# Performance work log

Hardware: AMD Instinct MI355X
Metric: run time of the kernel (lower is better)

The kernel has to match this reference:

```python
import jax, jax.numpy as jnp
import numpy as np
from math import sqrt

NUM_HEAD = 16
HEAD_DIM = 64  # out_dim // num_head = 1024 // 16


def setup_inputs() -> dict:
    key = jax.random.key(0)
    ks = jax.random.split(key, 6)
    B, L, D = 2, 2048, 1024
    s = 1.0 / sqrt(D)
    return {
        "x": jax.random.normal(ks[0], (B, L, D), jnp.float32),
        "position_embedding": jax.random.normal(ks[1], (1, NUM_HEAD, L, L), jnp.float32),
        "Wq": jax.random.normal(ks[2], (D, D), jnp.float32) * s,
        "Wk": jax.random.normal(ks[3], (D, D), jnp.float32) * s,
        "Wv": jax.random.normal(ks[4], (D, D), jnp.float32) * s,
        "Wo": jax.random.normal(ks[5], (D, D), jnp.float32) * s,
    }


def reference(x, position_embedding, Wq, Wk, Wv, Wo):
    # x: [B, L, D]; torch Linear(y = x @ W.T) -> here weights stored as [in, out]
    B, L, D = x.shape
    H, Hd = NUM_HEAD, HEAD_DIM
    q = (x @ Wq).reshape(B, L, H, Hd).transpose(0, 2, 1, 3)  # [B,H,L,Hd]
    k = (x @ Wk).reshape(B, L, H, Hd).transpose(0, 2, 1, 3)
    v = (x @ Wv).reshape(B, L, H, Hd).transpose(0, 2, 1, 3)
    scores = jnp.einsum("bhqd,bhkd->bhqk", q, k) / sqrt(Hd)  # [B,H,L,L]
    scores = scores + position_embedding
    attn = jax.nn.softmax(scores, axis=-1)
    out = jnp.einsum("bhqk,bhkd->bhqd", attn, v)  # [B,H,L,Hd]
    out = out.transpose(0, 2, 1, 3).reshape(B, L, H * Hd)
    return out @ Wo
```

## Files before the change

kernel.cpp:

```cpp
#include <hip/hip_runtime.h>
#include <hip/hip_bf16.h>
#include <stdint.h>

typedef __hip_bfloat16 bf16;
typedef __attribute__((ext_vector_type(8))) short bf16x8;
typedef __attribute__((ext_vector_type(4))) float f32x4;
typedef __attribute__((ext_vector_type(16))) float f32x16;
typedef __attribute__((ext_vector_type(4))) unsigned u32x4;

#define B_  2
#define L_  2048
#define D_  1024
#define H_  16
#define HD_ 64
#define BH_ 32
#define L2E 1.4426950408889634f

#define DEV static __device__ __forceinline__

DEV short f2bf(float f) {
    bf16 h = __float2bfloat16(f);
    return __builtin_bit_cast(short, h);
}

DEV unsigned pk2(float lo, float hi) {
    unsigned a = (unsigned short)__builtin_bit_cast(unsigned short, __float2bfloat16(lo));
    unsigned b = (unsigned short)__builtin_bit_cast(unsigned short, __float2bfloat16(hi));
    return a | (b << 16);
}

DEV f32x4 mfma16(bf16x8 a, bf16x8 b, f32x4 c) {
    return __builtin_amdgcn_mfma_f32_16x16x32_bf16(a, b, c, 0, 0, 0);
}
DEV f32x16 mfma32(bf16x8 a, bf16x8 b, f32x16 c) {
    return __builtin_amdgcn_mfma_f32_32x32x16_bf16(a, b, c, 0, 0, 0);
}

DEV void async_ld16(const void* g, void* lds_uniform) {
    __builtin_amdgcn_global_load_lds((const __attribute__((address_space(1))) void*)g,
                                     (__attribute__((address_space(3))) void*)lds_uniform,
                                     16, 0, 0);
}

DEV int swz(int row, int col) {
    int blk = (row << 3) + (col >> 3);
    blk ^= (row & 7);
    return (blk << 3) + (col & 7);
}

__global__ __launch_bounds__(256) void k_cast_x(const float* __restrict__ x,
                                                bf16* __restrict__ xb, int n8) {
    int i = blockIdx.x * 256 + threadIdx.x;
    if (i >= n8) return;
    const float4* src = (const float4*)x + (size_t)i * 2;
    float4 a = src[0], b = src[1];
    bf16x8 v;
    v[0]=f2bf(a.x); v[1]=f2bf(a.y); v[2]=f2bf(a.z); v[3]=f2bf(a.w);
    v[4]=f2bf(b.x); v[5]=f2bf(b.y); v[6]=f2bf(b.z); v[7]=f2bf(b.w);
    *(bf16x8*)(xb + (size_t)i * 8) = v;
}

__global__ __launch_bounds__(256) void k_cast_wT(const float* __restrict__ W0, const float* __restrict__ W1,
                                                 const float* __restrict__ W2, const float* __restrict__ W3,
                                                 bf16* __restrict__ WT) {
    const float* W = (blockIdx.z == 0) ? W0 : (blockIdx.z == 1) ? W1 : (blockIdx.z == 2) ? W2 : W3;
    __shared__ float tile[64][65];
    const int r0 = blockIdx.y * 64, c0 = blockIdx.x * 64;
    const int tx = threadIdx.x & 63, ty = threadIdx.x >> 6;
    #pragma unroll
    for (int i = 0; i < 16; ++i) {
        int r = ty + i * 4;
        tile[r][tx] = W[(size_t)(r0 + r) * D_ + c0 + tx];
    }
    __syncthreads();
    bf16* out = WT + (size_t)blockIdx.z * D_ * D_;
    #pragma unroll
    for (int i = 0; i < 16; ++i) {
        int n = ty + i * 4;
        out[(size_t)(c0 + n) * D_ + r0 + tx] = __float2bfloat16(tile[tx][n]);
    }
}

template <int MODE>
__global__ __launch_bounds__(256) void k_gemm(const bf16* __restrict__ A, const bf16* __restrict__ BT,
                                              void* __restrict__ C) {
    __shared__ __align__(16) bf16 As[128 * 64];
    __shared__ __align__(16) bf16 Bs[128 * 64];
    const int t = threadIdx.x;
    const int w = t >> 6, lane = t & 63;
    const int lr = lane & 15, lg = lane >> 4;
    const int wr = (w >> 1) * 64, wc = (w & 1) * 64;
    const size_t am0 = (size_t)blockIdx.y * 128;
    const size_t bn0 = (size_t)blockIdx.x * 128;

    f32x4 acc[4][4] = {};

    for (int kt = 0; kt < 1024 / 64; ++kt) {
        const int k0 = kt * 64;
        if (kt) __syncthreads();
        #pragma unroll
        for (int c = 0; c < 4; ++c) {
            int phys = c * 256 + t;
            int lb = phys ^ ((phys >> 3) & 7);
            int row = lb >> 3, cb = lb & 7;
            int ldsoff = (c * 256 + w * 64) * 8;
            async_ld16(A  + (am0 + row) * 1024 + k0 + cb * 8, (void*)(As + ldsoff));
            async_ld16(BT + (bn0 + row) * 1024 + k0 + cb * 8, (void*)(Bs + ldsoff));
        }
        __syncthreads();
        bf16x8 af[4][2], bfv[4][2];
        #pragma unroll
        for (int mi = 0; mi < 4; ++mi)
            #pragma unroll
            for (int ks = 0; ks < 2; ++ks)
                af[mi][ks] = *(const bf16x8*)(As + swz(wr + mi * 16 + lr, ks * 32 + lg * 8));
        #pragma unroll
        for (int ni = 0; ni < 4; ++ni)
            #pragma unroll
            for (int ks = 0; ks < 2; ++ks)
                bfv[ni][ks] = *(const bf16x8*)(Bs + swz(wc + ni * 16 + lr, ks * 32 + lg * 8));
        #pragma unroll
        for (int mi = 0; mi < 4; ++mi)
            #pragma unroll
            for (int ni = 0; ni < 4; ++ni) {
                acc[mi][ni] = mfma16(af[mi][0], bfv[ni][0], acc[mi][ni]);
                acc[mi][ni] = mfma16(af[mi][1], bfv[ni][1], acc[mi][ni]);
            }
    }

    #pragma unroll
    for (int mi = 0; mi < 4; ++mi)
        #pragma unroll
        for (int ni = 0; ni < 4; ++ni)
            #pragma unroll
            for (int j = 0; j < 4; ++j) {
                size_t gm = am0 + wr + mi * 16 + lg * 4 + j;
                size_t gn = bn0 + wc + ni * 16 + lr;
                float v = acc[mi][ni][j];
                if (MODE == 0) {
                    int which = (int)(gn >> 10);
                    int h = (int)((gn >> 6) & 15);
                    int d = (int)(gn & 63);
                    int bb = (int)(gm >> 11);
                    int l = (int)(gm & 2047);
                    if (which == 0) v *= 0.18033688011112042f;
                    bf16* dst = (bf16*)C + (size_t)which * ((size_t)BH_ * L_ * HD_);
                    dst[((size_t)(bb * H_ + h) * L_ + l) * HD_ + d] = __float2bfloat16(v);
                } else {
                    ((float*)C)[gm * 1024 + gn] = v;
                }
            }
}

__global__ __launch_bounds__(256) void k_transpose_v(const bf16* __restrict__ Vb, bf16* __restrict__ VTb) {
    __shared__ __align__(16) short tile[64][80];
    const int bh = blockIdx.y;
    const int l0 = blockIdx.x * 64;
    const int t = threadIdx.x;
    const int rr = t >> 2, cc = (t & 3) * 16;
    const short* src = (const short*)(Vb + ((size_t)bh * L_ + l0 + rr) * HD_ + cc);
    *(bf16x8*)&tile[rr][cc]     = *(const bf16x8*)src;
    *(bf16x8*)&tile[rr][cc + 8] = *(const bf16x8*)(src + 8);
    __syncthreads();
    bf16x8 v0, v1;
    #pragma unroll
    for (int i = 0; i < 8; ++i) v0[i] = tile[cc + i][rr];
    #pragma unroll
    for (int i = 0; i < 8; ++i) v1[i] = tile[cc + 8 + i][rr];
    short* dst = (short*)(VTb + ((size_t)bh * HD_ + rr) * L_ + l0 + cc);
    *(bf16x8*)dst       = v0;
    *(bf16x8*)(dst + 8) = v1;
}

__global__ __launch_bounds__(128, 1) void k_attn(const bf16* __restrict__ Qb, const bf16* __restrict__ Kb,
                                                 const bf16* __restrict__ VTb, const float* __restrict__ PE,
                                                 bf16* __restrict__ Ob) {
    __shared__ __align__(16) bf16 Kls[2][2][64 * 64];
    __shared__ __align__(16) bf16 Vls[2][2][64 * 64];

    const int bid = blockIdx.x;
    const int sw  = (bid & 7) * 64 + (bid >> 3);
    const int qt  = sw & 31, h = sw >> 5;
    const int q0  = qt * 64;
    const int t   = threadIdx.x;
    const int w   = t >> 6;
    const int l   = t & 63;
    const int lq  = l & 31;
    const int lh  = l >> 5;

    const int pb = (lq >> 2) & 3;
    const int prow = lq + (pb == 1 ? 4 : (pb == 2 ? -4 : 0));

    bf16x8 Qf[2][4];
    #pragma unroll
    for (int bi = 0; bi < 2; ++bi)
        #pragma unroll
        for (int dm = 0; dm < 4; ++dm)
            Qf[bi][dm] = *(const bf16x8*)(Qb + ((size_t)(bi * H_ + h) * L_ + q0 + w * 32 + lq) * HD_ + dm * 16 + lh * 8);

    const bf16* kb[2] = { Kb  + (size_t)(0 * H_ + h) * L_ * HD_,
                          Kb  + (size_t)(1 * H_ + h) * L_ * HD_ };
    const bf16* vb[2] = { VTb + (size_t)(0 * H_ + h) * HD_ * L_,
                          VTb + (size_t)(1 * H_ + h) * HD_ * L_ };
    const float* perow = PE + ((size_t)h * L_ + q0 + w * 32 + lq) * L_;

    int peoff[4];
    #pragma unroll
    for (int g = 0; g < 4; ++g)
        peoff[g] = (g >> 1) * 16 + (g & 1) * 4 + lh * 8;

    int srow[4], sblk[4];
    #pragma unroll
    for (int c = 0; c < 4; ++c) {
        int s = c * 128 + t;
        srow[c] = s >> 3;
        sblk[c] = (s & 7) ^ (srow[c] & 7);
    }

    int kro[2][4];
    #pragma unroll
    for (int ks = 0; ks < 2; ++ks)
        #pragma unroll
        for (int dm = 0; dm < 4; ++dm) {
            int R = ks * 32 + prow, cb = dm * 2 + lh;
            kro[ks][dm] = R * 64 + ((cb ^ (R & 7)) * 8);
        }
    int vro[2][2][2];
    #pragma unroll
    for (int ks = 0; ks < 2; ++ks)
        #pragma unroll
        for (int d0 = 0; d0 < 2; ++d0)
            #pragma unroll
            for (int m = 0; m < 2; ++m) {
                int R = d0 * 32 + lq, cb = ks * 4 + m * 2 + lh;
                vro[ks][d0][m] = R * 64 + ((cb ^ (R & 7)) * 8);
            }

    f32x16 o[2][2] = {};
    float mrun[2] = { -3e38f, -3e38f };
    float lpart[2] = { 0.f, 0.f };
    float4 peE[8], peO[8];

#define STAGE(BUF, TILE) {                                                              \
    _Pragma("unroll") for (int c = 0; c < 4; ++c) {                                     \
        async_ld16(kb[0] + (size_t)((TILE) * 64 + srow[c]) * HD_ + sblk[c] * 8,         \
                   (void*)(&Kls[BUF][0][0] + (c * 128 + w * 64) * 8));                  \
        async_ld16(kb[1] + (size_t)((TILE) * 64 + srow[c]) * HD_ + sblk[c] * 8,         \
                   (void*)(&Kls[BUF][1][0] + (c * 128 + w * 64) * 8));                  \
        async_ld16(vb[0] + (size_t)srow[c] * L_ + (TILE) * 64 + sblk[c] * 8,            \
                   (void*)(&Vls[BUF][0][0] + (c * 128 + w * 64) * 8));                  \
        async_ld16(vb[1] + (size_t)srow[c] * L_ + (TILE) * 64 + sblk[c] * 8,            \
                   (void*)(&Vls[BUF][1][0] + (c * 128 + w * 64) * 8));                  \
    }                                                                                   \
}

#define PELOAD(DST, TILE) {                                                             \
    _Pragma("unroll") for (int u = 0; u < 8; ++u)                                       \
        DST[u] = *(const float4*)(perow + (size_t)(TILE) * 64 + (u >> 2) * 32 + peoff[u & 3]); \
}

#define COMPUTE32(BI, KS, PEA, KL, VL) {                                                \
    bf16x8 kf0_ = *(const bf16x8*)((KL) + kro[KS][0]);                                  \
    bf16x8 kf1_ = *(const bf16x8*)((KL) + kro[KS][1]);                                  \
    bf16x8 kf2_ = *(const bf16x8*)((KL) + kro[KS][2]);                                  \
    bf16x8 kf3_ = *(const bf16x8*)((KL) + kro[KS][3]);                                  \
    f32x16 s = {};                                                                      \
    s = mfma32(kf0_, Qf[BI][0], s);                                                     \
    s = mfma32(kf1_, Qf[BI][1], s);                                                     \
    s = mfma32(kf2_, Qf[BI][2], s);                                                     \
    s = mfma32(kf3_, Qf[BI][3], s);                                                     \
    float v_[16];                                                                       \
    _Pragma("unroll") for (int r = 0; r < 16; ++r)                                      \
        v_[r] = fmaf(PEA[(KS) * 4 + (r >> 2)][r & 3], L2E, s[r]);                       \
    float t0_ = fmaxf(fmaxf(v_[0], v_[1]), fmaxf(v_[2], v_[3]));                        \
    float t1_ = fmaxf(fmaxf(v_[4], v_[5]), fmaxf(v_[6], v_[7]));                        \
    float t2_ = fmaxf(fmaxf(v_[8], v_[9]), fmaxf(v_[10], v_[11]));                      \
    float t3_ = fmaxf(fmaxf(v_[12], v_[13]), fmaxf(v_[14], v_[15]));                    \
    float vmh_ = fmaxf(fmaxf(t0_, t1_), fmaxf(t2_, t3_));                               \
    float vm_ = fmaxf(vmh_, __shfl_xor(vmh_, 32, 64));                                  \
    float mold_ = mrun[BI];                                                             \
    float mnew_ = mold_;                                                                \
    if (!__all(vm_ <= mold_ + 10.f)) {                                                  \
        mnew_ = fmaxf(mold_, vm_);                                                      \
        float scl_ = __builtin_amdgcn_exp2f(mold_ - mnew_);                             \
        mrun[BI] = mnew_;                                                               \
        lpart[BI] *= scl_;                                                              \
        _Pragma("unroll") for (int r = 0; r < 16; ++r) { o[BI][0][r] *= scl_; o[BI][1][r] *= scl_; } \
    }                                                                                   \
    float p_[16], ssum_ = 0.f;                                                          \
    _Pragma("unroll") for (int r = 0; r < 16; ++r) {                                    \
        p_[r] = __builtin_amdgcn_exp2f(v_[r] - mnew_);                                  \
        ssum_ += p_[r];                                                                 \
    }                                                                                   \
    lpart[BI] += ssum_;                                                                 \
    unsigned a_[8];                                                                     \
    _Pragma("unroll") for (int j = 0; j < 8; ++j)                                       \
        a_[j] = pk2(p_[2 * j], p_[2 * j + 1]);                                          \
    u32x4 w0v_ = { a_[0], a_[1], a_[2], a_[3] };                                        \
    u32x4 w1v_ = { a_[4], a_[5], a_[6], a_[7] };                                        \
    bf16x8 pf0_ = __builtin_bit_cast(bf16x8, w0v_);                                     \
    bf16x8 pf1_ = __builtin_bit_cast(bf16x8, w1v_);                                     \
    o[BI][0] = mfma32(*(const bf16x8*)((VL) + vro[KS][0][0]), pf0_, o[BI][0]);          \
    o[BI][0] = mfma32(*(const bf16x8*)((VL) + vro[KS][0][1]), pf1_, o[BI][0]);          \
    o[BI][1] = mfma32(*(const bf16x8*)((VL) + vro[KS][1][0]), pf0_, o[BI][1]);          \
    o[BI][1] = mfma32(*(const bf16x8*)((VL) + vro[KS][1][1]), pf1_, o[BI][1]);          \
}

#define HALF(BUF, PEA, TILE, PFT) {                                                     \
    COMPUTE32(0, 0, PEA, &Kls[BUF][0][0], &Vls[BUF][0][0])                              \
    COMPUTE32(0, 1, PEA, &Kls[BUF][0][0], &Vls[BUF][0][0])                              \
    COMPUTE32(1, 0, PEA, &Kls[BUF][1][0], &Vls[BUF][1][0])                              \
    COMPUTE32(1, 1, PEA, &Kls[BUF][1][0], &Vls[BUF][1][0])                              \
    PELOAD(PEA, PFT)                                                                    \
    __builtin_amdgcn_s_barrier();                                                       \
    STAGE(BUF, PFT)                                                                     \
    asm volatile("s_waitcnt vmcnt(24)" ::: "memory");                                   \
    __builtin_amdgcn_s_barrier();                                                       \
}

    STAGE(0, 0)
    STAGE(1, 1)
    PELOAD(peE, 0)
    PELOAD(peO, 1)
    asm volatile("s_waitcnt vmcnt(0)" ::: "memory");
    __builtin_amdgcn_s_barrier();

    for (int tp = 0; tp < 16; ++tp) {
        const int e = 2 * tp;
        const int pfA = (e + 2 < 32) ? e + 2 : 31;
        const int pfB = (e + 3 < 32) ? e + 3 : 31;
        HALF(0, peE, e, pfA)
        HALF(1, peO, e + 1, pfB)
    }
#undef HALF
#undef COMPUTE32
#undef PELOAD
#undef STAGE

    asm volatile("s_waitcnt vmcnt(0)" ::: "memory");

    #pragma unroll
    for (int bi = 0; bi < 2; ++bi) {
        float lsum = lpart[bi] + __shfl_xor(lpart[bi], 32, 64);
        float inv = __builtin_amdgcn_rcpf(lsum);
        #pragma unroll
        for (int d0 = 0; d0 < 2; ++d0)
            #pragma unroll
            for (int r = 0; r < 16; r += 2) {
                float e0 = o[bi][d0][r] * inv;
                float e1 = o[bi][d0][r + 1] * inv;
                int d = d0 * 32 + ((r & 3) + 8 * (r >> 2)) + lh * 4;
                *(unsigned*)(Ob + ((size_t)bi * L_ + q0 + w * 32 + lq) * D_ + h * HD_ + d) = pk2(e0, e1);
            }
    }
}

extern "C" void kernel_launch(void* const* d_in, const int* in_sizes, int n_in,
                              void* d_out, int out_size, void* d_ws, size_t ws_size,
                              hipStream_t stream) {
    const float* x  = (const float*)d_in[0];
    const float* pe = (const float*)d_in[1];
    const float* Wq = (const float*)d_in[2];
    const float* Wk = (const float*)d_in[3];
    const float* Wv = (const float*)d_in[4];
    const float* Wo = (const float*)d_in[5];
    float* out = (float*)d_out;

    const size_t MD = (size_t)4096 * 1024;
    const size_t HS = (size_t)BH_ * L_ * HD_;

    bf16* Xb  = (bf16*)d_ws;
    bf16* WT  = Xb + MD;
    bf16* Qb  = WT + MD;
    bf16* Kb  = Qb + HS;
    bf16* Vb  = Kb + HS;
    bf16* VTb = Vb + HS;
    bf16* Ob  = VTb + HS;

    k_cast_x<<<2048, 256, 0, stream>>>(x, Xb, 4096 * 1024 / 8);
    k_cast_wT<<<dim3(16, 16, 4), 256, 0, stream>>>(Wq, Wk, Wv, Wo, WT);
    k_gemm<0><<<dim3(24, 32), 256, 0, stream>>>(Xb, WT, (void*)Qb);
    k_transpose_v<<<dim3(32, 32), 256, 0, stream>>>(Vb, VTb);
    k_attn<<<512, 128, 0, stream>>>(Qb, Kb, VTb, pe, Ob);
    k_gemm<1><<<dim3(8, 32), 256, 0, stream>>>(Ob, WT + (size_t)3072 * 1024, (void*)out);
}
```

Baseline: 198.9 us.

## Split attention batches across waves and stage position embedding through LDS

The attention kernel moves from 2 waves, each handling both batch entries, to 4 waves, each owning one (batch, 32-query) slice. K/V tiles shrink to 32 keys per step over 64 iterations. The position-embedding tile is now loaded asynchronously into shared memory with a swizzled layout, shared by the two batch waves, instead of per-thread register prefetch. Launch bounds change to 256 threads with 3 blocks per CU to raise occupancy and cut register pressure, at the cost of more barriers and iterations per tile.

```diff
diff --git a/kernel.cpp b/kernel.cpp
--- a/kernel.cpp
+++ b/kernel.cpp
@@ -172,127 +172,115 @@
     *(bf16x8*)(dst + 8) = v1;
 }
 
-__global__ __launch_bounds__(128, 1) void k_attn(const bf16* __restrict__ Qb, const bf16* __restrict__ Kb,
+__global__ __launch_bounds__(256, 3) void k_attn(const bf16* __restrict__ Qb, const bf16* __restrict__ Kb,
                                                  const bf16* __restrict__ VTb, const float* __restrict__ PE,
                                                  bf16* __restrict__ Ob) {
-    __shared__ __align__(16) bf16 Kls[2][2][64 * 64];
-    __shared__ __align__(16) bf16 Vls[2][2][64 * 64];
+    __shared__ __align__(16) char shm[49152];
 
     const int bid = blockIdx.x;
     const int sw  = (bid & 7) * 64 + (bid >> 3);
     const int qt  = sw & 31, h = sw >> 5;
-    const int q0  = qt * 64;
     const int t   = threadIdx.x;
-    const int w   = t >> 6;
-    const int l   = t & 63;
+    const int w   = t >> 6, l = t & 63;
+    const int qs  = w & 1, b = w >> 1;
+    const int q0  = qt * 64 + qs * 32;
     const int lq  = l & 31;
     const int lh  = l >> 5;
 
     const int pb = (lq >> 2) & 3;
     const int prow = lq + (pb == 1 ? 4 : (pb == 2 ? -4 : 0));
 
-    bf16x8 Qf[2][4];
-    #pragma unroll
-    for (int bi = 0; bi < 2; ++bi)
-        #pragma unroll
-        for (int dm = 0; dm < 4; ++dm)
-            Qf[bi][dm] = *(const bf16x8*)(Qb + ((size_t)(bi * H_ + h) * L_ + q0 + w * 32 + lq) * HD_ + dm * 16 + lh * 8);
-
-    const bf16* kb[2] = { Kb  + (size_t)(0 * H_ + h) * L_ * HD_,
-                          Kb  + (size_t)(1 * H_ + h) * L_ * HD_ };
-    const bf16* vb[2] = { VTb + (size_t)(0 * H_ + h) * HD_ * L_,
-                          VTb + (size_t)(1 * H_ + h) * HD_ * L_ };
-    const float* perow = PE + ((size_t)h * L_ + q0 + w * 32 + lq) * L_;
-
-    int peoff[4];
+    bf16x8 Qf[4];
+    #pragma unroll
+    for (int dm = 0; dm < 4; ++dm)
+        Qf[dm] = *(const bf16x8*)(Qb + ((size_t)(b * H_ + h) * L_ + q0 + lq) * HD_ + dm * 16 + lh * 8);
+
+    const bf16*  kb  = Kb  + (size_t)(b * H_ + h) * L_ * HD_;
+    const bf16*  vbp = VTb + (size_t)(b * H_ + h) * HD_ * L_;
+    const float* peq = PE  + ((size_t)h * L_ + q0) * L_;
+
+    const int k_srcoff  = (l >> 3) * HD_ + (((l & 7) ^ (l >> 3)) * 8);
+    const int v_srcoff  = (l >> 2) * L_  + (((l & 3) ^ ((l >> 2) & 3)) * 8);
+    const int pe_srcoff = (l >> 3) * L_  + (((l & 7) ^ (l >> 3)) * 4);
+
+    int kro[4];
+    #pragma unroll
+    for (int dm = 0; dm < 4; ++dm)
+        kro[dm] = prow * 64 + (((dm * 2 + lh) ^ (prow & 7)) * 8);
+    int vro[2][2];
+    #pragma unroll
+    for (int d0 = 0; d0 < 2; ++d0)
+        #pragma unroll
+        for (int m = 0; m < 2; ++m)
+            vro[d0][m] = (d0 * 32 + lq) * 32 + (((m * 2 + lh) ^ (lq & 3)) * 8);
+    int peo[4];
     #pragma unroll
     for (int g = 0; g < 4; ++g)
-        peoff[g] = (g >> 1) * 16 + (g & 1) * 4 + lh * 8;
-
-    int srow[4], sblk[4];
-    #pragma unroll
-    for (int c = 0; c < 4; ++c) {
-        int s = c * 128 + t;
-        srow[c] = s >> 3;
-        sblk[c] = (s & 7) ^ (srow[c] & 7);
-    }
-
-    int kro[2][4];
-    #pragma unroll
-    for (int ks = 0; ks < 2; ++ks)
-        #pragma unroll
-        for (int dm = 0; dm < 4; ++dm) {
-            int R = ks * 32 + prow, cb = dm * 2 + lh;
-            kro[ks][dm] = R * 64 + ((cb ^ (R & 7)) * 8);
-        }
-    int vro[2][2][2];
-    #pragma unroll
-    for (int ks = 0; ks < 2; ++ks)
-        #pragma unroll
-        for (int d0 = 0; d0 < 2; ++d0)
-            #pragma unroll
-            for (int m = 0; m < 2; ++m) {
-                int R = d0 * 32 + lq, cb = ks * 4 + m * 2 + lh;
-                vro[ks][d0][m] = R * 64 + ((cb ^ (R & 7)) * 8);
-            }
-
-    f32x16 o[2][2] = {};
-    float mrun[2] = { -3e38f, -3e38f };
-    float lpart[2] = { 0.f, 0.f };
-    float4 peE[8], peO[8];
+        peo[g] = lq * 32 + ((((g >> 1) * 4 + (g & 1) + lh * 2) ^ (lq & 7)) * 4);
+
+#define SH_K(BUF)  (shm + (BUF) * 24576 + b * 4096)
+#define SH_V(BUF)  (shm + (BUF) * 24576 + 8192 + b * 4096)
+#define SH_PE(BUF) (shm + (BUF) * 24576 + 16384 + qs * 4096)
+
+    f32x16 o[2] = {};
+    float mrun = -3e38f, lpart = 0.f;
 
 #define STAGE(BUF, TILE) {                                                              \
-    _Pragma("unroll") for (int c = 0; c < 4; ++c) {                                     \
-        async_ld16(kb[0] + (size_t)((TILE) * 64 + srow[c]) * HD_ + sblk[c] * 8,         \
-                   (void*)(&Kls[BUF][0][0] + (c * 128 + w * 64) * 8));                  \
-        async_ld16(kb[1] + (size_t)((TILE) * 64 + srow[c]) * HD_ + sblk[c] * 8,         \
-                   (void*)(&Kls[BUF][1][0] + (c * 128 + w * 64) * 8));                  \
-        async_ld16(vb[0] + (size_t)srow[c] * L_ + (TILE) * 64 + sblk[c] * 8,            \
-                   (void*)(&Vls[BUF][0][0] + (c * 128 + w * 64) * 8));                  \
-        async_ld16(vb[1] + (size_t)srow[c] * L_ + (TILE) * 64 + sblk[c] * 8,            \
-                   (void*)(&Vls[BUF][1][0] + (c * 128 + w * 64) * 8));                  \
-    }                                                                                   \
-}
-
-#define PELOAD(DST, TILE) {                                                             \
-    _Pragma("unroll") for (int u = 0; u < 8; ++u)                                       \
-        DST[u] = *(const float4*)(perow + (size_t)(TILE) * 64 + (u >> 2) * 32 + peoff[u & 3]); \
-}
-
-#define COMPUTE32(BI, KS, PEA, KL, VL) {                                                \
-    bf16x8 kf0_ = *(const bf16x8*)((KL) + kro[KS][0]);                                  \
-    bf16x8 kf1_ = *(const bf16x8*)((KL) + kro[KS][1]);                                  \
-    bf16x8 kf2_ = *(const bf16x8*)((KL) + kro[KS][2]);                                  \
-    bf16x8 kf3_ = *(const bf16x8*)((KL) + kro[KS][3]);                                  \
+    const int kv0_ = (TILE) * 32;                                                       \
+    _Pragma("unroll") for (int i = 0; i < 2; ++i) {                                     \
+        const int c = 2 * qs + i;                                                       \
+        async_ld16(kb + (size_t)(kv0_ + c * 8) * HD_ + k_srcoff, (void*)(SH_K(BUF) + c * 1024)); \
+    }                                                                                   \
+    _Pragma("unroll") for (int i = 0; i < 2; ++i) {                                     \
+        const int c = 2 * qs + i;                                                       \
+        async_ld16(vbp + (size_t)(c * 16) * L_ + kv0_ + v_srcoff, (void*)(SH_V(BUF) + c * 1024)); \
+    }                                                                                   \
+    _Pragma("unroll") for (int i = 0; i < 2; ++i) {                                     \
+        const int c = 2 * b + i;                                                        \
+        async_ld16(peq + (size_t)(c * 8) * L_ + kv0_ + pe_srcoff, (void*)(SH_PE(BUF) + c * 1024)); \
+    }                                                                                   \
+}
+
+#define COMPUTE(BUF) {                                                                  \
+    const bf16*  KL = (const bf16*)SH_K(BUF);                                           \
+    const bf16*  VL = (const bf16*)SH_V(BUF);                                           \
+    const float* PL = (const float*)SH_PE(BUF);                                         \
+    bf16x8 kf0_ = *(const bf16x8*)(KL + kro[0]);                                        \
+    bf16x8 kf1_ = *(const bf16x8*)(KL + kro[1]);                                        \
+    bf16x8 kf2_ = *(const bf16x8*)(KL + kro[2]);                                        \
+    bf16x8 kf3_ = *(const bf16x8*)(KL + kro[3]);                                        \
     f32x16 s = {};                                                                      \
-    s = mfma32(kf0_, Qf[BI][0], s);                                                     \
-    s = mfma32(kf1_, Qf[BI][1], s);                                                     \
-    s = mfma32(kf2_, Qf[BI][2], s);                                                     \
-    s = mfma32(kf3_, Qf[BI][3], s);                                                     \
+    s = mfma32(kf0_, Qf[0], s);                                                         \
+    s = mfma32(kf1_, Qf[1], s);                                                         \
+    s = mfma32(kf2_, Qf[2], s);                                                         \
+    s = mfma32(kf3_, Qf[3], s);                                                         \
+    float4 pef_[4];                                                                     \
+    _Pragma("unroll") for (int g = 0; g < 4; ++g)                                       \
+        pef_[g] = *(const float4*)(PL + peo[g]);                                        \
     float v_[16];                                                                       \
     _Pragma("unroll") for (int r = 0; r < 16; ++r)                                      \
-        v_[r] = fmaf(PEA[(KS) * 4 + (r >> 2)][r & 3], L2E, s[r]);                       \
+        v_[r] = fmaf(pef_[r >> 2][r & 3], L2E, s[r]);                                   \
     float t0_ = fmaxf(fmaxf(v_[0], v_[1]), fmaxf(v_[2], v_[3]));                        \
     float t1_ = fmaxf(fmaxf(v_[4], v_[5]), fmaxf(v_[6], v_[7]));                        \
     float t2_ = fmaxf(fmaxf(v_[8], v_[9]), fmaxf(v_[10], v_[11]));                      \
     float t3_ = fmaxf(fmaxf(v_[12], v_[13]), fmaxf(v_[14], v_[15]));                    \
     float vmh_ = fmaxf(fmaxf(t0_, t1_), fmaxf(t2_, t3_));                               \
     float vm_ = fmaxf(vmh_, __shfl_xor(vmh_, 32, 64));                                  \
-    float mold_ = mrun[BI];                                                             \
+    float mold_ = mrun;                                                                 \
     float mnew_ = mold_;                                                                \
     if (!__all(vm_ <= mold_ + 10.f)) {                                                  \
         mnew_ = fmaxf(mold_, vm_);                                                      \
         float scl_ = __builtin_amdgcn_exp2f(mold_ - mnew_);                             \
-        mrun[BI] = mnew_;                                                               \
-        lpart[BI] *= scl_;                                                              \
-        _Pragma("unroll") for (int r = 0; r < 16; ++r) { o[BI][0][r] *= scl_; o[BI][1][r] *= scl_; } \
+        mrun = mnew_;                                                                   \
+        lpart *= scl_;                                                                  \
+        _Pragma("unroll") for (int r = 0; r < 16; ++r) { o[0][r] *= scl_; o[1][r] *= scl_; } \
     }                                                                                   \
     float p_[16], ssum_ = 0.f;                                                          \
     _Pragma("unroll") for (int r = 0; r < 16; ++r) {                                    \
         p_[r] = __builtin_amdgcn_exp2f(v_[r] - mnew_);                                  \
         ssum_ += p_[r];                                                                 \
     }                                                                                   \
-    lpart[BI] += ssum_;                                                                 \
+    lpart += ssum_;                                                                     \
     unsigned a_[8];                                                                     \
     _Pragma("unroll") for (int j = 0; j < 8; ++j)                                       \
         a_[j] = pk2(p_[2 * j], p_[2 * j + 1]);                                          \
@@ -300,59 +288,45 @@
     u32x4 w1v_ = { a_[4], a_[5], a_[6], a_[7] };                                        \
     bf16x8 pf0_ = __builtin_bit_cast(bf16x8, w0v_);                                     \
     bf16x8 pf1_ = __builtin_bit_cast(bf16x8, w1v_);                                     \
-    o[BI][0] = mfma32(*(const bf16x8*)((VL) + vro[KS][0][0]), pf0_, o[BI][0]);          \
-    o[BI][0] = mfma32(*(const bf16x8*)((VL) + vro[KS][0][1]), pf1_, o[BI][0]);          \
-    o[BI][1] = mfma32(*(const bf16x8*)((VL) + vro[KS][1][0]), pf0_, o[BI][1]);          \
-    o[BI][1] = mfma32(*(const bf16x8*)((VL) + vro[KS][1][1]), pf1_, o[BI][1]);          \
-}
-
-#define HALF(BUF, PEA, TILE, PFT) {                                                     \
-    COMPUTE32(0, 0, PEA, &Kls[BUF][0][0], &Vls[BUF][0][0])                              \
-    COMPUTE32(0, 1, PEA, &Kls[BUF][0][0], &Vls[BUF][0][0])                              \
-    COMPUTE32(1, 0, PEA, &Kls[BUF][1][0], &Vls[BUF][1][0])                              \
-    COMPUTE32(1, 1, PEA, &Kls[BUF][1][0], &Vls[BUF][1][0])                              \
-    PELOAD(PEA, PFT)                                                                    \
-    __builtin_amdgcn_s_barrier();                                                       \
-    STAGE(BUF, PFT)                                                                     \
-    asm volatile("s_waitcnt vmcnt(24)" ::: "memory");                                   \
-    __builtin_amdgcn_s_barrier();                                                       \
+    o[0] = mfma32(*(const bf16x8*)(VL + vro[0][0]), pf0_, o[0]);                        \
+    o[0] = mfma32(*(const bf16x8*)(VL + vro[0][1]), pf1_, o[0]);                        \
+    o[1] = mfma32(*(const bf16x8*)(VL + vro[1][0]), pf0_, o[1]);                        \
+    o[1] = mfma32(*(const bf16x8*)(VL + vro[1][1]), pf1_, o[1]);                        \
 }
 
     STAGE(0, 0)
     STAGE(1, 1)
-    PELOAD(peE, 0)
-    PELOAD(peO, 1)
+    asm volatile("s_waitcnt vmcnt(6)" ::: "memory");
+    __builtin_amdgcn_s_barrier();
+
+    for (int tt = 0; tt < 64; ++tt) {
+        const int buf = tt & 1;
+        if (buf == 0) { COMPUTE(0) } else { COMPUTE(1) }
+        __builtin_amdgcn_s_barrier();
+        const int pft = (tt + 2 < 64) ? tt + 2 : 63;
+        if (buf == 0) { STAGE(0, pft) } else { STAGE(1, pft) }
+        asm volatile("s_waitcnt vmcnt(6)" ::: "memory");
+        __builtin_amdgcn_s_barrier();
+    }
+#undef COMPUTE
+#undef STAGE
+#undef SH_K
+#undef SH_V
+#undef SH_PE
+
     asm volatile("s_waitcnt vmcnt(0)" ::: "memory");
-    __builtin_amdgcn_s_barrier();
-
-    for (int tp = 0; tp < 16; ++tp) {
-        const int e = 2 * tp;
-        const int pfA = (e + 2 < 32) ? e + 2 : 31;
-        const int pfB = (e + 3 < 32) ? e + 3 : 31;
-        HALF(0, peE, e, pfA)
-        HALF(1, peO, e + 1, pfB)
-    }
-#undef HALF
-#undef COMPUTE32
-#undef PELOAD
-#undef STAGE
-
-    asm volatile("s_waitcnt vmcnt(0)" ::: "memory");
-
-    #pragma unroll
-    for (int bi = 0; bi < 2; ++bi) {
-        float lsum = lpart[bi] + __shfl_xor(lpart[bi], 32, 64);
-        float inv = __builtin_amdgcn_rcpf(lsum);
-        #pragma unroll
-        for (int d0 = 0; d0 < 2; ++d0)
-            #pragma unroll
-            for (int r = 0; r < 16; r += 2) {
-                float e0 = o[bi][d0][r] * inv;
-                float e1 = o[bi][d0][r + 1] * inv;
-                int d = d0 * 32 + ((r & 3) + 8 * (r >> 2)) + lh * 4;
-                *(unsigned*)(Ob + ((size_t)bi * L_ + q0 + w * 32 + lq) * D_ + h * HD_ + d) = pk2(e0, e1);
-            }
-    }
+
+    float lsum = lpart + __shfl_xor(lpart, 32, 64);
+    float inv = __builtin_amdgcn_rcpf(lsum);
+    #pragma unroll
+    for (int d0 = 0; d0 < 2; ++d0)
+        #pragma unroll
+        for (int r = 0; r < 16; r += 2) {
+            float e0 = o[d0][r] * inv;
+            float e1 = o[d0][r + 1] * inv;
+            int d = d0 * 32 + ((r & 3) + 8 * (r >> 2)) + lh * 4;
+            *(unsigned*)(Ob + ((size_t)b * L_ + q0 + lq) * D_ + h * HD_ + d) = pk2(e0, e1);
+        }
 }
 
 extern "C" void kernel_launch(void* const* d_in, const int* in_sizes, int n_in,
@@ -381,6 +355,6 @@
     k_cast_wT<<<dim3(16, 16, 4), 256, 0, stream>>>(Wq, Wk, Wv, Wo, WT);
     k_gemm<0><<<dim3(24, 32), 256, 0, stream>>>(Xb, WT, (void*)Qb);
     k_transpose_v<<<dim3(32, 32), 256, 0, stream>>>(Vb, VTb);
-    k_attn<<<512, 128, 0, stream>>>(Qb, Kb, VTb, pe, Ob);
+    k_attn<<<512, 256, 0, stream>>>(Qb, Kb, VTb, pe, Ob);
     k_gemm<1><<<dim3(8, 32), 256, 0, stream>>>(Ob, WT + (size_t)3072 * 1024, (void*)out);
 }
```

Result: faster. 172.9 us (-13.0%).
